# Optimization experiments

Measured on AMD Instinct MI355X. Metric: run time of the kernel, lower is better.

## Reference

```python
import jax, jax.numpy as jnp
import numpy as np

D_MODEL = 1024
HEADS = 16
D_K = D_MODEL // HEADS
MAX_LEN = 2048
SCALE = 1.0 / np.sqrt(D_K)


def setup_inputs() -> dict:
    key = jax.random.key(0)
    ks = jax.random.split(key, 12)
    S, B = 2048, 2
    lin = lambda k: jax.random.normal(k, (D_MODEL, D_MODEL), jnp.float32) * (1.0 / np.sqrt(D_MODEL))
    return {
        "query": jax.random.normal(ks[0], (S, B, D_MODEL), jnp.float32),
        "key": jax.random.normal(ks[1], (S, B, D_MODEL), jnp.float32),
        "value": jax.random.normal(ks[2], (S, B, D_MODEL), jnp.float32),
        "Wq": lin(ks[3]), "bq": jnp.zeros((D_MODEL,), jnp.float32),
        "Wk": lin(ks[4]), "bk": jnp.zeros((D_MODEL,), jnp.float32),
        "Wv": lin(ks[5]), "bv": jnp.zeros((D_MODEL,), jnp.float32),
        "Wo": lin(ks[6]), "bo": jnp.zeros((D_MODEL,), jnp.float32),
        "rel_table": jax.random.normal(ks[7], (2 * MAX_LEN - 1, HEADS), jnp.float32),
    }


def reference(query, key, value, Wq, bq, Wk, bk, Wv, bv, Wo, bo, rel_table):
    q_len, B, _ = query.shape
    k_len = key.shape[0]
    # projections (torch Linear: x @ W.T + b)
    q = (query @ Wq.T + bq).reshape(q_len, B, HEADS, D_K)
    k = (key @ Wk.T + bk).reshape(k_len, B, HEADS, D_K)
    v = (value @ Wv.T + bv).reshape(k_len, B, HEADS, D_K)
    scores = jnp.einsum('qbhd,kbhd->bhqk', q, k) * SCALE
    # relative position bias gather
    dist = jnp.arange(q_len)[:, None] - jnp.arange(k_len)[None, :] + (MAX_LEN - 1)
    dist = jnp.clip(dist, 0, 2 * MAX_LEN - 2)
    bias = rel_table[dist]                     # [q,k,h]
    scores = scores + jnp.transpose(bias, (2, 0, 1))[None]  # [1,h,q,k]
    attn = jax.nn.softmax(scores, axis=-1)
    out = jnp.einsum('bhqk,kbhd->qbhd', attn, v).reshape(q_len, B, D_MODEL)
    return out @ Wo.T + bo
```

## Files before the change

kernel.cpp:

```cpp
#include <hip/hip_runtime.h>
#include <hip/hip_bf16.h>

typedef __bf16 bf16_t;
typedef __bf16 bf16x8 __attribute__((ext_vector_type(8)));
typedef __bf16 bf16x4 __attribute__((ext_vector_type(4)));
typedef float f32x4 __attribute__((ext_vector_type(4)));

#define D_MODEL 1024
#define HEADS 16
#define D_K 64
#define SEQ 2048
#define BATCH 2
#define MTOT (SEQ * BATCH)
#define LOG2E 1.4426950408889634f
#define QSCALE (0.125f * LOG2E)

#define GLDS16(g, l)                                                        \
  __builtin_amdgcn_global_load_lds(                                        \
      (const __attribute__((address_space(1))) unsigned int*)(g),          \
      (__attribute__((address_space(3))) unsigned int*)(l), 16, 0, 0)

__global__ __launch_bounds__(256) void cvt4_kernel(const float* s0, const float* s1,
                                                   const float* s2, const float* s3,
                                                   bf16_t* d0, bf16_t* d1, bf16_t* d2,
                                                   bf16_t* d3, int n) {
  const float* s; bf16_t* d;
  switch (blockIdx.y) {
    case 0: s = s0; d = d0; break;
    case 1: s = s1; d = d1; break;
    case 2: s = s2; d = d2; break;
    default: s = s3; d = d3; break;
  }
  int i = (blockIdx.x * 256 + threadIdx.x) * 8;
  if (i >= n) return;
  float4 a = *(const float4*)(s + i);
  float4 b = *(const float4*)(s + i + 4);
  bf16x8 v;
  v[0] = (bf16_t)a.x; v[1] = (bf16_t)a.y; v[2] = (bf16_t)a.z; v[3] = (bf16_t)a.w;
  v[4] = (bf16_t)b.x; v[5] = (bf16_t)b.y; v[6] = (bf16_t)b.z; v[7] = (bf16_t)b.w;
  *(bf16x8*)(d + i) = v;
}

__global__ __launch_bounds__(256, 3) void gemm_qkv(const bf16_t* __restrict__ Xq,
                                                   const bf16_t* __restrict__ Xk,
                                                   const bf16_t* __restrict__ Xv,
                                                   const bf16_t* __restrict__ Wqkv,
                                                   const float* __restrict__ bq,
                                                   const float* __restrict__ bk,
                                                   const float* __restrict__ bv,
                                                   bf16_t* __restrict__ qa,
                                                   bf16_t* __restrict__ ka,
                                                   bf16_t* __restrict__ vt) {
  __shared__ __align__(16) bf16_t As[2][128 * 64];
  const int t = threadIdx.x;
  const int f = blockIdx.x;
  const int xcd = f & 7, fi = f >> 3;
  const int by = xcd * 4 + (fi & 3);
  const int col = fi >> 2;
  const int seg = col >> 3;
  const bf16_t* X = seg == 0 ? Xq : (seg == 1 ? Xk : Xv);
  const float* bias = seg == 0 ? bq : (seg == 1 ? bk : bv);
  const float scale = seg == 0 ? QSCALE : 1.0f;
  const int m0 = by * 128;
  const int n0g = col * 128;
  const int w = t >> 6, l = t & 63, lr = l & 15, lg = l >> 4;
  const int wm = (w >> 1) * 64, wn = (w & 1) * 64;

  f32x4 acc[4][4] = {};

  const int srow0 = t >> 3;
  const int sck = (((t & 7) ^ (srow0 & 7)) << 3);
  const int sx = (lr & 7) << 4;

  const bf16_t* Wp = Wqkv + (size_t)(n0g + wn + lr) * D_MODEL + lg * 8;

#define QKV_STAGE(buf, kt)                                                    \
  {                                                                           \
    _Pragma("unroll") for (int p = 0; p < 4; ++p) {                           \
      int row = (p * 256 + t) >> 3;                                           \
      int wb = (p * 256 + w * 64) * 8;                                        \
      GLDS16(&X[(size_t)(m0 + row) * D_MODEL + (kt) + sck], As[buf] + wb);    \
    }                                                                         \
  }

  QKV_STAGE(0, 0);
  __syncthreads();

  for (int step = 0; step < 16; ++step) {
    const int cur = step & 1;
    const int kt = step * 64;
    if (step + 1 < 16) QKV_STAGE(cur ^ 1, kt + 64);
#pragma unroll
    for (int kk = 0; kk < 2; ++kk) {
      bf16x8 a[4], b[4];
#pragma unroll
      for (int i = 0; i < 4; ++i)
        a[i] = *(const bf16x8*)((const char*)As[cur] + (wm + i * 16 + lr) * 128 +
                                ((kk * 64 + lg * 16) ^ sx));
#pragma unroll
      for (int j = 0; j < 4; ++j)
        b[j] = *(const bf16x8*)(Wp + (size_t)j * 16 * D_MODEL + kt + kk * 32);
#pragma unroll
      for (int i = 0; i < 4; ++i)
#pragma unroll
        for (int j = 0; j < 4; ++j)
          acc[i][j] = __builtin_amdgcn_mfma_f32_16x16x32_bf16(a[i], b[j], acc[i][j], 0, 0, 0);
    }
    __syncthreads();
  }
#undef QKV_STAGE

#pragma unroll
  for (int i = 0; i < 4; ++i) {
#pragma unroll
    for (int j = 0; j < 4; ++j) {
      int lc = ((n0g + wn) & 1023) + j * 16 + lr;
      float bb = bias[lc];
      int h = lc >> 6, d = lc & 63;
#pragma unroll
      for (int ii = 0; ii < 4; ++ii) {
        int row = m0 + wm + i * 16 + lg * 4 + ii;
        float v = (acc[i][j][ii] + bb) * scale;
        int s = row >> 1, b2 = row & 1;
        if (seg == 2)
          vt[(((size_t)(b2 * HEADS + h) * D_K) + d) * SEQ + s] = (bf16_t)v;
        else if (seg == 1)
          ka[(((size_t)(b2 * HEADS + h) * SEQ) + s) * D_K + d] = (bf16_t)v;
        else
          qa[(((size_t)(b2 * HEADS + h) * SEQ) + s) * D_K + d] = (bf16_t)v;
      }
    }
  }
}

__global__ __launch_bounds__(512) void gemm_out(const bf16_t* __restrict__ X,
                                                const bf16_t* __restrict__ W,
                                                const float* __restrict__ bias,
                                                float* __restrict__ out) {
  __shared__ __align__(16) bf16_t As[2][128 * 64];
  __shared__ __align__(16) bf16_t Bs[2][128 * 64];
  const int t = threadIdx.x;
  const int f = blockIdx.x;
  const int xcd = f & 7, fi = f >> 3;
  const int by = xcd * 4 + (fi & 3);
  const int bx = fi >> 2;
  const int m0 = by * 128, n0 = bx * 128;
  const int w = t >> 6, l = t & 63, lr = l & 15, lg = l >> 4;
  const int wm = (w >> 2) * 64, wn = (w & 3) * 32;
  const int srow0 = t >> 3;
  const int sck = (((t & 7) ^ (srow0 & 7)) << 3);
  const int sx = (lr & 7) << 4;

  f32x4 acc[4][2] = {};

#define OUT_STAGE(buf, kt)                                                      \
  {                                                                             \
    _Pragma("unroll") for (int p = 0; p < 2; ++p) {                             \
      int row = (p * 512 + t) >> 3;                                             \
      int wb = (p * 512 + w * 64) * 8;                                          \
      GLDS16(&X[(size_t)(m0 + row) * D_MODEL + (kt) + sck], As[buf] + wb);      \
      GLDS16(&W[(size_t)(n0 + row) * D_MODEL + (kt) + sck], Bs[buf] + wb);      \
    }                                                                           \
  }

  OUT_STAGE(0, 0);
  __syncthreads();

  for (int step = 0; step < 16; ++step) {
    const int cur = step & 1;
    if (step + 1 < 16) OUT_STAGE(cur ^ 1, (step + 1) * 64);
#pragma unroll
    for (int kk = 0; kk < 2; ++kk) {
      bf16x8 a[4], b[2];
#pragma unroll
      for (int i = 0; i < 4; ++i)
        a[i] = *(const bf16x8*)((const char*)As[cur] + (wm + i * 16 + lr) * 128 +
                                ((kk * 64 + lg * 16) ^ sx));
#pragma unroll
      for (int j = 0; j < 2; ++j)
        b[j] = *(const bf16x8*)((const char*)Bs[cur] + (wn + j * 16 + lr) * 128 +
                                ((kk * 64 + lg * 16) ^ sx));
#pragma unroll
      for (int i = 0; i < 4; ++i)
#pragma unroll
        for (int j = 0; j < 2; ++j)
          acc[i][j] = __builtin_amdgcn_mfma_f32_16x16x32_bf16(a[i], b[j], acc[i][j], 0, 0, 0);
    }
    __syncthreads();
  }
#undef OUT_STAGE

#pragma unroll
  for (int i = 0; i < 4; ++i) {
#pragma unroll
    for (int j = 0; j < 2; ++j) {
      int col = n0 + wn + j * 16 + lr;
      float bb = bias[col];
#pragma unroll
      for (int ii = 0; ii < 4; ++ii) {
        int row = m0 + wm + i * 16 + lg * 4 + ii;
        out[(size_t)row * D_MODEL + col] = acc[i][j][ii] + bb;
      }
    }
  }
}

#define QBLK 128
#define KVBLK 64
#define NT (SEQ / KVBLK)
#define TBL_N 2175
#define LDP 72

__global__ __launch_bounds__(512, 4) void attn_kernel(const bf16_t* __restrict__ Qa,
                                                      const bf16_t* __restrict__ Ka,
                                                      const bf16_t* __restrict__ Vt,
                                                      const float* __restrict__ rel,
                                                      bf16_t* __restrict__ ctx) {
  __shared__ float rbl[TBL_N + 1];
  __shared__ __align__(16) bf16_t ks[2][KVBLK * 64];
  __shared__ __align__(16) bf16_t vs[2][KVBLK * 64];
  __shared__ __align__(16) bf16_t p_lds[8][16 * LDP];

  const int f = blockIdx.x;
  const int nf = (f & 7) * 64 + (f >> 3);
  const int qb = nf & 15, bh = nf >> 4;
  const int h = bh & (HEADS - 1), b2 = bh >> 4;
  const int qbase = qb * QBLK;
  const int t = threadIdx.x, w = t >> 6, l = t & 63, lr = l & 15, lg = l >> 4;

  const bf16_t* Qbh = Qa + (size_t)bh * SEQ * D_K;
  const bf16_t* Kbh = Ka + (size_t)bh * SEQ * D_K;
  const bf16_t* Vbh = Vt + (size_t)bh * D_K * SEQ;

  for (int j = t; j < TBL_N; j += 512)
    rbl[j] = LOG2E * rel[(size_t)(qbase + (TBL_N - 1) - j) * HEADS + h];

  const int srow = t >> 3;
  const int scol = (((t & 7) ^ (srow & 7)) << 3);
  const int sldsoff = w * 512;

  const int qloc = w * 16 + lr;
  bf16x8 qf[2];
#pragma unroll
  for (int kk = 0; kk < 2; ++kk)
    qf[kk] = *(const bf16x8*)(&Qbh[(size_t)(qbase + qloc) * D_K + kk * 32 + lg * 8]);

  bf16x8 ones;
#pragma unroll
  for (int e = 0; e < 8; ++e) ones[e] = (bf16_t)1.0f;

  GLDS16(Kbh + (size_t)srow * D_K + scol, ks[0] + sldsoff);
  GLDS16(Vbh + (size_t)srow * SEQ + scol, vs[0] + sldsoff);
  __syncthreads();

  f32x4 acc_o[4] = {};
  f32x4 l_acc = {};
  bf16_t* pw = p_lds[w];
  const int sw = (lr & 7) << 4;
  const int roff = 127 - qloc + lg * 4;

  for (int it = 0; it < NT; ++it) {
    const int cur = it & 1;
    const int kt = it * KVBLK;
    if (it + 1 < NT) {
      const int ktn = kt + KVBLK;
      GLDS16(Kbh + (size_t)(ktn + srow) * D_K + scol, ks[cur ^ 1] + sldsoff);
      GLDS16(Vbh + (size_t)srow * SEQ + ktn + scol, vs[cur ^ 1] + sldsoff);
    }
    const char* Kc = (const char*)ks[cur];
    const char* Vc = (const char*)vs[cur];

#pragma unroll
    for (int c = 0; c < 4; ++c) {
      const int r0 = roff + kt + c * 16;
      f32x4 z;
      z[0] = rbl[r0]; z[1] = rbl[r0 + 1]; z[2] = rbl[r0 + 2]; z[3] = rbl[r0 + 3];
#pragma unroll
      for (int kk = 0; kk < 2; ++kk) {
        bf16x8 kf = *(const bf16x8*)(Kc + (c * 16 + lr) * 128 + ((kk * 64 + lg * 16) ^ sw));
        z = __builtin_amdgcn_mfma_f32_16x16x32_bf16(kf, qf[kk], z, 0, 0, 0);
      }
      bf16x4 pv;
#pragma unroll
      for (int i = 0; i < 4; ++i) pv[i] = (bf16_t)__builtin_amdgcn_exp2f(z[i]);
      *(bf16x4*)(&pw[lr * LDP + c * 16 + lg * 4]) = pv;
    }

    __builtin_amdgcn_s_setprio(1);
#pragma unroll
    for (int kk = 0; kk < 2; ++kk) {
      bf16x8 pa = *(const bf16x8*)(&pw[lr * LDP + kk * 32 + lg * 8]);
      l_acc = __builtin_amdgcn_mfma_f32_16x16x32_bf16(ones, pa, l_acc, 0, 0, 0);
#pragma unroll
      for (int c = 0; c < 4; ++c) {
        bf16x8 vf = *(const bf16x8*)(Vc + (c * 16 + lr) * 128 + ((kk * 64 + lg * 16) ^ sw));
        acc_o[c] = __builtin_amdgcn_mfma_f32_16x16x32_bf16(vf, pa, acc_o[c], 0, 0, 0);
      }
    }
    __builtin_amdgcn_s_setprio(0);
    __syncthreads();
  }

  const float inv = 1.0f / l_acc[0];

  int qg = qbase + qloc;
  size_t base = ((size_t)qg * BATCH + b2) * D_MODEL + h * D_K;
#pragma unroll
  for (int c = 0; c < 4; ++c) {
    bf16x4 ov;
#pragma unroll
    for (int ii = 0; ii < 4; ++ii) ov[ii] = (bf16_t)(acc_o[c][ii] * inv);
    *(bf16x4*)(&ctx[base + c * 16 + lg * 4]) = ov;
  }
}

extern "C" void kernel_launch(void* const* d_in, const int* in_sizes, int n_in,
                              void* d_out, int out_size, void* d_ws, size_t ws_size,
                              hipStream_t stream) {
  const float* query = (const float*)d_in[0];
  const float* key_i = (const float*)d_in[1];
  const float* value = (const float*)d_in[2];
  const float* Wq = (const float*)d_in[3];
  const float* bq = (const float*)d_in[4];
  const float* Wk = (const float*)d_in[5];
  const float* bk = (const float*)d_in[6];
  const float* Wv = (const float*)d_in[7];
  const float* bv = (const float*)d_in[8];
  const float* Wo = (const float*)d_in[9];
  const float* bo = (const float*)d_in[10];
  const float* rel = (const float*)d_in[11];
  float* out = (float*)d_out;

  char* ws = (char*)d_ws;
  size_t off = 0;
  auto alloc = [&](size_t bytes) {
    char* p = ws + off;
    off = (off + bytes + 255) & ~(size_t)255;
    return p;
  };
  const size_t nIn = (size_t)MTOT * D_MODEL;
  const size_t nW = (size_t)D_MODEL * D_MODEL;

  bf16_t* Xq = (bf16_t*)alloc(nIn * 2);
  bf16_t* Xk = (bf16_t*)alloc(nIn * 2);
  bf16_t* Xv = (bf16_t*)alloc(nIn * 2);
  bf16_t* Wqkv = (bf16_t*)alloc(3 * nW * 2);
  bf16_t* Wob = (bf16_t*)alloc(nW * 2);
  bf16_t* qa = (bf16_t*)alloc(nIn * 2);
  bf16_t* ka = (bf16_t*)alloc(nIn * 2);
  bf16_t* vt = (bf16_t*)alloc(nIn * 2);
  bf16_t* ctx = (bf16_t*)alloc(nIn * 2);

  cvt4_kernel<<<dim3(nIn / 2048, 3), 256, 0, stream>>>(query, key_i, value, value, Xq, Xk,
                                                       Xv, Xv, (int)nIn);
  cvt4_kernel<<<dim3(nW / 2048, 4), 256, 0, stream>>>(Wq, Wk, Wv, Wo, Wqkv, Wqkv + nW,
                                                      Wqkv + 2 * nW, Wob, (int)nW);

  gemm_qkv<<<dim3(768), 256, 0, stream>>>(Xq, Xk, Xv, Wqkv, bq, bk, bv, qa, ka, vt);

  attn_kernel<<<dim3(512), 512, 0, stream>>>(qa, ka, vt, rel, ctx);

  gemm_out<<<dim3(256), 512, 0, stream>>>(ctx, Wob, bo, out);
}
```

Before: 148.6 us.

## Drop LDS staging in QKV GEMM, load A directly into registers with double-buffering

The QKV projection GEMM no longer stages the activation tile through LDS with async global-to-LDS loads and barriers. Each wave now loads its A and B fragments straight from global memory into registers and double-buffers them in a two-chunk software pipeline. This removes LDS traffic and __syncthreads, at the cost of duplicated global/L2 reads of A across the two waves sharing rows and higher register pressure.

```diff
diff --git a/kernel.cpp b/kernel.cpp
--- a/kernel.cpp
+++ b/kernel.cpp
@@ -51,7 +51,6 @@
                                                    bf16_t* __restrict__ qa,
                                                    bf16_t* __restrict__ ka,
                                                    bf16_t* __restrict__ vt) {
-  __shared__ __align__(16) bf16_t As[2][128 * 64];
   const int t = threadIdx.x;
   const int f = blockIdx.x;
   const int xcd = f & 7, fi = f >> 3;
@@ -66,49 +65,36 @@
   const int w = t >> 6, l = t & 63, lr = l & 15, lg = l >> 4;
   const int wm = (w >> 1) * 64, wn = (w & 1) * 64;
 
+  const bf16_t* Ap = X + (size_t)(m0 + wm + lr) * D_MODEL + lg * 8;
+  const bf16_t* Bp = Wqkv + (size_t)(n0g + wn + lr) * D_MODEL + lg * 8;
+
   f32x4 acc[4][4] = {};
-
-  const int srow0 = t >> 3;
-  const int sck = (((t & 7) ^ (srow0 & 7)) << 3);
-  const int sx = (lr & 7) << 4;
-
-  const bf16_t* Wp = Wqkv + (size_t)(n0g + wn + lr) * D_MODEL + lg * 8;
-
-#define QKV_STAGE(buf, kt)                                                    \
-  {                                                                           \
-    _Pragma("unroll") for (int p = 0; p < 4; ++p) {                           \
-      int row = (p * 256 + t) >> 3;                                           \
-      int wb = (p * 256 + w * 64) * 8;                                        \
-      GLDS16(&X[(size_t)(m0 + row) * D_MODEL + (kt) + sck], As[buf] + wb);    \
-    }                                                                         \
-  }
-
-  QKV_STAGE(0, 0);
-  __syncthreads();
-
-  for (int step = 0; step < 16; ++step) {
-    const int cur = step & 1;
-    const int kt = step * 64;
-    if (step + 1 < 16) QKV_STAGE(cur ^ 1, kt + 64);
-#pragma unroll
-    for (int kk = 0; kk < 2; ++kk) {
-      bf16x8 a[4], b[4];
-#pragma unroll
-      for (int i = 0; i < 4; ++i)
-        a[i] = *(const bf16x8*)((const char*)As[cur] + (wm + i * 16 + lr) * 128 +
-                                ((kk * 64 + lg * 16) ^ sx));
-#pragma unroll
-      for (int j = 0; j < 4; ++j)
-        b[j] = *(const bf16x8*)(Wp + (size_t)j * 16 * D_MODEL + kt + kk * 32);
-#pragma unroll
-      for (int i = 0; i < 4; ++i)
-#pragma unroll
-        for (int j = 0; j < 4; ++j)
-          acc[i][j] = __builtin_amdgcn_mfma_f32_16x16x32_bf16(a[i], b[j], acc[i][j], 0, 0, 0);
-    }
-    __syncthreads();
-  }
-#undef QKV_STAGE
+  bf16x8 a0[4], b0[4], a1[4], b1[4];
+
+#define LOADC(A, B, koff)                                                   \
+  {                                                                         \
+    _Pragma("unroll") for (int i = 0; i < 4; ++i)                           \
+        A[i] = *(const bf16x8*)(Ap + (size_t)i * 16 * D_MODEL + (koff));    \
+    _Pragma("unroll") for (int j = 0; j < 4; ++j)                           \
+        B[j] = *(const bf16x8*)(Bp + (size_t)j * 16 * D_MODEL + (koff));    \
+  }
+#define MFMAC(A, B)                                                         \
+  {                                                                         \
+    _Pragma("unroll") for (int i = 0; i < 4; ++i)                           \
+        _Pragma("unroll") for (int j = 0; j < 4; ++j)                       \
+            acc[i][j] =                                                     \
+        __builtin_amdgcn_mfma_f32_16x16x32_bf16(A[i], B[j], acc[i][j], 0, 0, 0); \
+  }
+
+  LOADC(a0, b0, 0);
+  for (int c = 0; c < 32; c += 2) {
+    if (c + 1 < 32) LOADC(a1, b1, (c + 1) * 32);
+    MFMAC(a0, b0);
+    if (c + 2 < 32) LOADC(a0, b0, (c + 2) * 32);
+    MFMAC(a1, b1);
+  }
+#undef LOADC
+#undef MFMAC
 
 #pragma unroll
   for (int i = 0; i < 4; ++i) {
```

After: 181.6 us. 1.22x slower.
